# Kernel tuning notes

Measured on AMD Instinct MI355X. Metric: run time of the kernel, lower is better.

Reference implementation:

```python
import jax, jax.numpy as jnp
import numpy as np
from jax import lax

T, N, E = 12, 20000, 320000          # timesteps, nodes/graph, edges/graph
F_IN, H_GCN, H_LSTM, N_CLS = 128, 256, 256, 8
NUM_GRAPHS = 1                        # one graph per snapshot (batch all zeros)


def setup_inputs() -> dict:
    key = jax.random.key(0)
    ks = jax.random.split(key, 12)
    s = 0.05
    return {
        "x": jax.random.normal(ks[0], (T, N, F_IN), jnp.float32),
        "edge_index": jax.random.randint(ks[1], (T, 2, E), 0, N, dtype=jnp.int32),
        "batch": jnp.zeros((T, N), jnp.int32),
        "W1": jax.random.normal(ks[2], (F_IN, H_GCN), jnp.float32) * s,
        "b1": jnp.zeros((H_GCN,), jnp.float32),
        "W2": jax.random.normal(ks[3], (H_GCN, H_GCN), jnp.float32) * s,
        "b2": jnp.zeros((H_GCN,), jnp.float32),
        "Wih0": jax.random.normal(ks[4], (4 * H_LSTM, H_GCN), jnp.float32) * s,
        "Whh0": jax.random.normal(ks[5], (4 * H_LSTM, H_LSTM), jnp.float32) * s,
        "bih0": jnp.zeros((4 * H_LSTM,), jnp.float32),
        "bhh0": jnp.zeros((4 * H_LSTM,), jnp.float32),
        "Wih1": jax.random.normal(ks[6], (4 * H_LSTM, H_LSTM), jnp.float32) * s,
        "Whh1": jax.random.normal(ks[7], (4 * H_LSTM, H_LSTM), jnp.float32) * s,
        "bih1": jnp.zeros((4 * H_LSTM,), jnp.float32),
        "bhh1": jnp.zeros((4 * H_LSTM,), jnp.float32),
        "Wlin": jax.random.normal(ks[8], (N_CLS, H_LSTM), jnp.float32) * s,
        "blin": jnp.zeros((N_CLS,), jnp.float32),
    }


def gcn_conv(x, src, dst, W, b, n):
    """PyG GCNConv: linear -> add self-loops -> sym-norm gather/scale/scatter-add + bias."""
    loop = jnp.arange(n, dtype=src.dtype)
    src = jnp.concatenate([src, loop])
    dst = jnp.concatenate([dst, loop])
    deg = jax.ops.segment_sum(jnp.ones(dst.shape, x.dtype), dst, num_segments=n)
    dinv = jnp.where(deg > 0, lax.rsqrt(deg), 0.0)
    norm = dinv[src] * dinv[dst]                       # [E+N]
    xl = x @ W                                         # [N, H]
    out = jax.ops.segment_sum(xl[src] * norm[:, None], dst, num_segments=n)
    return out + b


def lstm_layer(xs, Wih, Whh, bih, bhh):
    """Single-direction LSTM over xs [T, D]; PyTorch gate order i,f,g,o."""
    H = Whh.shape[1]
    bias = bih + bhh

    def step(carry, x):
        h, c = carry
        gates = x @ Wih.T + h @ Whh.T + bias
        i, f, g, o = jnp.split(gates, 4, axis=-1)
        c = jax.nn.sigmoid(f) * c + jax.nn.sigmoid(i) * jnp.tanh(g)
        h = jax.nn.sigmoid(o) * jnp.tanh(c)
        return (h, c), h

    h0 = jnp.zeros((H,), xs.dtype)
    (_, _), hs = lax.scan(step, (h0, h0), xs)
    return hs


def reference(x, edge_index, batch, W1, b1, W2, b2,
              Wih0, Whh0, bih0, bhh0, Wih1, Whh1, bih1, bhh1, Wlin, blin):
    def gcn_step(_, inp):
        xt, et, bt = inp
        h = jax.nn.relu(gcn_conv(xt, et[0], et[1], W1, b1, N))
        h = jax.nn.relu(gcn_conv(h, et[0], et[1], W2, b2, N))
        sums = jax.ops.segment_sum(h, bt, num_segments=NUM_GRAPHS)
        cnt = jax.ops.segment_sum(jnp.ones((N,), h.dtype), bt, num_segments=NUM_GRAPHS)
        return 0, sums / cnt[:, None]                  # global_mean_pool -> [NUM_GRAPHS, H_GCN]

    _, pooled = lax.scan(gcn_step, 0, (x, edge_index, batch))
    seq = pooled.reshape(T * NUM_GRAPHS, H_GCN)        # cat(dim=0) of per-step embeddings
    h1 = lstm_layer(seq, Wih0, Whh0, bih0, bhh0)
    h2 = lstm_layer(h1, Wih1, Whh1, bih1, bhh1)
    return (h2[-1] @ Wlin.T + blin)[None, :]           # [1, N_CLS]
```

## Files before the change

### kernel.cpp

```cpp
#include <hip/hip_runtime.h>
#include <hip/hip_bf16.h>
#include <math.h>

#define T_STEPS 12
#define NNODES  20000
#define NEDGES  320000
#define MPAD    20032
#define FIN     128
#define HG      256
#define RS_STRIDE 20032
#define CHK     16
#define HALF    10000

typedef unsigned short u16;
typedef unsigned int   u32;
typedef unsigned char  u8;
typedef unsigned long long u64;
using bf16x8 = __attribute__((ext_vector_type(8))) short;
using f32x4  = __attribute__((ext_vector_type(4))) float;
typedef float v2f __attribute__((ext_vector_type(2)));

__device__ __forceinline__ float bf2f(u16 u) {
    union { u32 i; float f; } v; v.i = ((u32)u) << 16; return v.f;
}
__device__ __forceinline__ u16 f2bf(float f) {
    union { float f; u32 i; } v; v.f = f;
    u32 r = v.i + 0x7fffu + ((v.i >> 16) & 1u);
    return (u16)(r >> 16);
}
__device__ __forceinline__ u16 f2h(float f) {
    _Float16 h = (_Float16)f; u16 u; __builtin_memcpy(&u, &h, 2); return u;
}
__device__ __forceinline__ float h2f(u16 u) {
    _Float16 h; __builtin_memcpy(&h, &u, 2); return (float)h;
}
__device__ __forceinline__ void gload16(const void* g, void* l) {
    __builtin_amdgcn_global_load_lds(
        (const __attribute__((address_space(1))) u32*)g,
        (__attribute__((address_space(3))) u32*)l, 16, 0, 0);
}
__device__ __forceinline__ float sigm(float x) { return 1.f / (1.f + expf(-x)); }


__global__ void __launch_bounds__(1024) hist2(const int* __restrict__ edges,
        u8* __restrict__ rank, u8* __restrict__ counts) {
    __shared__ u32 lh[HALF];
    int c = blockIdx.x & 15;
    int rest = blockIdx.x >> 4;
    int s = rest & 1, t = rest >> 1;
    for (int i = threadIdx.x; i < HALF; i += 1024) lh[i] = 0;
    __syncthreads();
    int lo = s * HALF;
    const int* db = edges + (size_t)t * 2 * NEDGES + NEDGES;
    u8* rk = rank + (size_t)t * NEDGES;
    int per = NEDGES / CHK;
    int e0 = c * per, e1 = e0 + per;
    for (int i = e0 + (int)threadIdx.x; i < e1; i += 1024) {
        int d = db[i] - lo;
        if ((unsigned)d < HALF) {
            u32 r = atomicAdd(&lh[d], 1u);
            rk[i] = (u8)r;
        }
    }
    __syncthreads();
    u8* cnt = counts + (((size_t)(t * 2 + s) * CHK + c) * HALF);
    for (int i = threadIdx.x; i < HALF; i += 1024) cnt[i] = (u8)lh[i];
}

__global__ void __launch_bounds__(1024) scan2(const u8* __restrict__ counts,
        int* __restrict__ rowstart, float* __restrict__ dinv,
        int* __restrict__ chunkoff) {
    int t = blockIdx.x;
    int tid = threadIdx.x;
    int wid = tid >> 6, lane = tid & 63;
    __shared__ int wsum[16];
    __shared__ int carry_s;
    if (tid == 0) carry_s = 0;
    __syncthreads();
    for (int base = 0; base < NNODES; base += 1024) {
        int i = base + tid;
        int cl[CHK];
        int orig = 0;
        if (i < NNODES) {
            int s = i / HALF, np = i - s * HALF;
            const u8* cp = counts + ((size_t)(t * 2 + s) * CHK) * HALF + np;
#pragma unroll
            for (int c = 0; c < CHK; ++c) { cl[c] = cp[c * HALF]; orig += cl[c]; }
        }
        int v = orig;
#pragma unroll
        for (int off = 1; off < 64; off <<= 1) {
            int n = __shfl_up(v, off);
            if (lane >= off) v += n;
        }
        if (lane == 63) wsum[wid] = v;
        __syncthreads();
        if (wid == 0 && lane < 16) {
            int s = wsum[lane];
#pragma unroll
            for (int off = 1; off < 16; off <<= 1) {
                int n = __shfl_up(s, off);
                if (lane >= off) s += n;
            }
            wsum[lane] = s;
        }
        __syncthreads();
        int incl = v + (wid > 0 ? wsum[wid - 1] : 0) + carry_s;
        int excl = incl - orig;
        if (i < NNODES) {
            rowstart[t * RS_STRIDE + i] = excl;
            dinv[t * NNODES + i] = rsqrtf((float)(orig + 1));
            int s = i / HALF, np = i - s * HALF;
            int* op = chunkoff + ((size_t)(t * 2 + s) * CHK) * HALF + np;
            int run = excl;
#pragma unroll
            for (int c = 0; c < CHK; ++c) { op[c * HALF] = run; run += cl[c]; }
        }
        __syncthreads();
        if (tid == 0) carry_s += wsum[15];
        __syncthreads();
    }
    if (tid == 0) rowstart[t * RS_STRIDE + NNODES] = carry_s;
}

__global__ void __launch_bounds__(1024) fill2(const int* __restrict__ edges,
        const u8* __restrict__ rank, const int* __restrict__ chunkoff,
        int* __restrict__ col) {
    __shared__ int loff[HALF];
    int c = blockIdx.x & 15;
    int rest = blockIdx.x >> 4;
    int s = rest & 1, t = rest >> 1;
    const int* op = chunkoff + (((size_t)(t * 2 + s) * CHK + c) * HALF);
    for (int i = threadIdx.x; i < HALF; i += 1024) loff[i] = op[i];
    __syncthreads();
    int lo = s * HALF;
    const int* sb = edges + (size_t)t * 2 * NEDGES;
    const int* db = sb + NEDGES;
    const u8* rk = rank + (size_t)t * NEDGES;
    int* ct = col + (size_t)t * NEDGES;
    int per = NEDGES / CHK;
    int e0 = c * per, e1 = e0 + per;
    for (int i = e0 + (int)threadIdx.x; i < e1; i += 1024) {
        int d = db[i] - lo;
        if ((unsigned)d < HALF)
            ct[loff[d] + (int)rk[i]] = sb[i];
    }
}


__global__ void __launch_bounds__(256) convall(
        const float* __restrict__ x, const float* __restrict__ dinv, u8* __restrict__ xb,
        const float* __restrict__ W1, u16* __restrict__ W1t,
        const float* __restrict__ W2, u16* __restrict__ W2t,
        const float* __restrict__ Wih0, const float* __restrict__ Whh0,
        const float* __restrict__ Wih1, const float* __restrict__ Whh1,
        u32* __restrict__ lw,
        float* __restrict__ pooled, u64* __restrict__ hbuf) {
    int bid = blockIdx.x;
    int tid = threadIdx.x;
    if (bid < 30000) {
        int idx = bid * 256 + tid;
        int row = idx >> 5, q = idx & 31;
        float dn = dinv[row];
        float4 v = *(const float4*)&x[(size_t)row * FIN + q * 4];
        int p = __builtin_amdgcn_cvt_pk_fp8_f32(dn * v.x, dn * v.y, 0, false);
        p = __builtin_amdgcn_cvt_pk_fp8_f32(dn * v.z, dn * v.w, p, true);
        ((u32*)xb)[(size_t)row * 32 + q] = (u32)p;
    } else if (bid < 30128) {
        int idx = (bid - 30000) * 256 + tid;
        int n = idx / FIN, k = idx - n * FIN;
        W1t[idx] = f2bf(W1[k * HG + n]);
    } else if (bid < 30384) {
        int idx = (bid - 30128) * 256 + tid;
        int n = idx >> 8, k = idx & 255;
        W2t[idx] = f2bf(W2[k * HG + n]);
    } else if (bid == 30384) {
        for (int i = tid; i < T_STEPS * HG; i += 256) pooled[i] = 0.f;
        for (int i = tid; i < 256; i += 256) hbuf[i] = 0ull;
    } else {
        int idx = bid - 30385;
        int m = idx >> 10, r = idx & 1023;
        const float* src = (m == 0) ? Wih0 : (m == 1) ? Whh0 : (m == 2) ? Wih1 : Whh1;
        if (tid < 128) {
            float2 w2 = *(const float2*)&src[(size_t)r * HG + tid * 2];
            lw[((size_t)m * 128 + tid) * 1024 + r] =
                (u32)f2h(w2.x) | ((u32)f2h(w2.y) << 16);
        }
    }
}


__global__ void __launch_bounds__(256) agg128(const u8* __restrict__ xb,
        const int* __restrict__ rowstart, const int* __restrict__ col,
        const float* __restrict__ dinv, u16* __restrict__ out) {
    int glob = (blockIdx.x << 2) + (threadIdx.x >> 6);
    int lane = threadIdx.x & 63;
    int t = glob / MPAD, node = glob - t * MPAD;
    u16* orow = out + ((size_t)glob) * FIN;
    if (node >= NNODES) { *(u32*)&orow[lane << 1] = 0; return; }
    const u8* xt = xb + (size_t)t * NNODES * FIN;
    const int* cb = col + (size_t)t * NEDGES;
    int o2 = lane << 1;
    u32 pv = *(const u16*)&xt[(size_t)node * FIN + o2];
    v2f f = __builtin_amdgcn_cvt_pk_f32_fp8((int)pv, false);
    float ax = f[0], ay = f[1];
    int s0 = rowstart[t * RS_STRIDE + node], s1 = rowstart[t * RS_STRIDE + node + 1];
    int e = s0;
    for (; e + 16 <= s1; e += 16) {
        int ix[16]; u32 rv[16];
#pragma unroll
        for (int j = 0; j < 16; ++j) ix[j] = cb[e + j];
#pragma unroll
        for (int j = 0; j < 16; ++j) rv[j] = *(const u16*)&xt[(size_t)ix[j] * FIN + o2];
#pragma unroll
        for (int j = 0; j < 16; ++j) {
            v2f g = __builtin_amdgcn_cvt_pk_f32_fp8((int)rv[j], false);
            ax += g[0]; ay += g[1];
        }
    }
    for (; e + 4 <= s1; e += 4) {
        int ix[4]; u32 rv[4];
#pragma unroll
        for (int j = 0; j < 4; ++j) ix[j] = cb[e + j];
#pragma unroll
        for (int j = 0; j < 4; ++j) rv[j] = *(const u16*)&xt[(size_t)ix[j] * FIN + o2];
#pragma unroll
        for (int j = 0; j < 4; ++j) {
            v2f g = __builtin_amdgcn_cvt_pk_f32_fp8((int)rv[j], false);
            ax += g[0]; ay += g[1];
        }
    }
    for (; e < s1; ++e) {
        u32 rv = *(const u16*)&xt[(size_t)cb[e] * FIN + o2];
        v2f g = __builtin_amdgcn_cvt_pk_f32_fp8((int)rv, false);
        ax += g[0]; ay += g[1];
    }
    float dn = dinv[t * NNODES + node];
    u32 packed = (u32)f2bf(dn * ax) | ((u32)f2bf(dn * ay) << 16);
    *(u32*)&orow[o2] = packed;
}

__global__ void __launch_bounds__(256) agg256(const u8* __restrict__ xin,
        const int* __restrict__ rowstart, const int* __restrict__ col,
        const float* __restrict__ dinv, u16* __restrict__ out) {
    int glob = (blockIdx.x << 2) + (threadIdx.x >> 6);
    int lane = threadIdx.x & 63;
    int t = glob / MPAD, node = glob - t * MPAD;
    u16* orow = out + ((size_t)glob) * HG;
    if (node >= NNODES) { *(ushort4*)&orow[lane << 2] = make_ushort4(0, 0, 0, 0); return; }
    const u8* xt = xin + (size_t)t * MPAD * HG;
    const int* cb = col + (size_t)t * NEDGES;
    int o4 = lane << 2;
    u32 pv = *(const u32*)&xt[(size_t)node * HG + o4];
    v2f f01 = __builtin_amdgcn_cvt_pk_f32_fp8((int)pv, false);
    v2f f23 = __builtin_amdgcn_cvt_pk_f32_fp8((int)pv, true);
    float a0 = f01[0], a1 = f01[1], a2 = f23[0], a3 = f23[1];
    int s0 = rowstart[t * RS_STRIDE + node], s1 = rowstart[t * RS_STRIDE + node + 1];
    int e = s0;
    for (; e + 16 <= s1; e += 16) {
        int ix[16]; u32 rv[16];
#pragma unroll
        for (int j = 0; j < 16; ++j) ix[j] = cb[e + j];
#pragma unroll
        for (int j = 0; j < 16; ++j) rv[j] = *(const u32*)&xt[(size_t)ix[j] * HG + o4];
#pragma unroll
        for (int j = 0; j < 16; ++j) {
            v2f g01 = __builtin_amdgcn_cvt_pk_f32_fp8((int)rv[j], false);
            v2f g23 = __builtin_amdgcn_cvt_pk_f32_fp8((int)rv[j], true);
            a0 += g01[0]; a1 += g01[1]; a2 += g23[0]; a3 += g23[1];
        }
    }
    for (; e + 4 <= s1; e += 4) {
        int ix[4]; u32 rv[4];
#pragma unroll
        for (int j = 0; j < 4; ++j) ix[j] = cb[e + j];
#pragma unroll
        for (int j = 0; j < 4; ++j) rv[j] = *(const u32*)&xt[(size_t)ix[j] * HG + o4];
#pragma unroll
        for (int j = 0; j < 4; ++j) {
            v2f g01 = __builtin_amdgcn_cvt_pk_f32_fp8((int)rv[j], false);
            v2f g23 = __builtin_amdgcn_cvt_pk_f32_fp8((int)rv[j], true);
            a0 += g01[0]; a1 += g01[1]; a2 += g23[0]; a3 += g23[1];
        }
    }
    for (; e < s1; ++e) {
        u32 rv = *(const u32*)&xt[(size_t)cb[e] * HG + o4];
        v2f g01 = __builtin_amdgcn_cvt_pk_f32_fp8((int)rv, false);
        v2f g23 = __builtin_amdgcn_cvt_pk_f32_fp8((int)rv, true);
        a0 += g01[0]; a1 += g01[1]; a2 += g23[0]; a3 += g23[1];
    }
    float dn = dinv[t * NNODES + node];
    ushort4 o;
    o.x = f2bf(dn * a0); o.y = f2bf(dn * a1); o.z = f2bf(dn * a2); o.w = f2bf(dn * a3);
    *(ushort4*)&orow[o4] = o;
}


template <int K, bool POOL>
__global__ __launch_bounds__(256) void gemm_bf16(
        const u16* __restrict__ A, const u16* __restrict__ Bt,
        const float* __restrict__ bias, const float* __restrict__ dscale,
        u8* __restrict__ C, float* __restrict__ pool) {
    __shared__ u16 As[64 * 64];
    __shared__ u16 Bs[256 * 64];
    __shared__ float csum[HG];
    int tid = threadIdx.x;
    int bm = blockIdx.x * 64;
    int t8 = tid >> 3, sl = tid & 7;
    int lane = tid & 63, w = tid >> 6;
    int r0 = lane & 15, gq = lane >> 4;
    int tblk = blockIdx.x / 313;

    f32x4 acc[4][4] = {};

    for (int k0 = 0; k0 < K; k0 += 64) {
#pragma unroll
        for (int i = 0; i < 2; ++i) {
            int r = i * 32 + t8;
            int ch = sl ^ (r & 7);
            gload16(A + (size_t)(bm + r) * K + k0 + ch * 8, &As[i * 2048 + tid * 8]);
        }
#pragma unroll
        for (int i = 0; i < 8; ++i) {
            int r = i * 32 + t8;
            int ch = sl ^ (r & 7);
            gload16(Bt + (size_t)r * K + k0 + ch * 8, &Bs[i * 2048 + tid * 8]);
        }
        __syncthreads();
#pragma unroll
        for (int kk = 0; kk < 2; ++kk) {
            bf16x8 a[4], b[4];
#pragma unroll
            for (int mi = 0; mi < 4; ++mi) {
                int R = mi * 16 + r0;
                int s = (kk * 4 + gq) ^ (R & 7);
                a[mi] = *(const bf16x8*)&As[R * 64 + s * 8];
            }
#pragma unroll
            for (int ni = 0; ni < 4; ++ni) {
                int R = w * 64 + ni * 16 + r0;
                int s = (kk * 4 + gq) ^ (R & 7);
                b[ni] = *(const bf16x8*)&Bs[R * 64 + s * 8];
            }
#pragma unroll
            for (int mi = 0; mi < 4; ++mi)
#pragma unroll
                for (int ni = 0; ni < 4; ++ni)
                    acc[mi][ni] = __builtin_amdgcn_mfma_f32_16x16x32_bf16(
                        a[mi], b[ni], acc[mi][ni], 0, 0, 0);
        }
        __syncthreads();
    }

    if (!POOL) {
#pragma unroll
        for (int ni = 0; ni < 4; ++ni) {
            int colg = w * 64 + ni * 16 + r0;
            float b = bias[colg];
#pragma unroll
            for (int mi = 0; mi < 4; ++mi) {
                int rbase = bm + mi * 16 + gq * 4;
#pragma unroll
                for (int q = 0; q < 4; ++q) {
                    int row = rbase + q;
                    int rloc = row - tblk * MPAD;
                    float sc = (rloc < NNODES) ? dscale[tblk * NNODES + rloc] : 0.f;
                    float val = sc * fmaxf(acc[mi][ni][q] + b, 0.f);
                    int p = __builtin_amdgcn_cvt_pk_fp8_f32(val, val, 0, false);
                    C[(size_t)row * HG + colg] = (u8)(p & 0xff);
                }
            }
        }
    } else {
        csum[tid] = 0.f;
        __syncthreads();
#pragma unroll
        for (int ni = 0; ni < 4; ++ni) {
            int colg = w * 64 + ni * 16 + r0;
            float b = bias[colg];
            float s = 0.f;
#pragma unroll
            for (int mi = 0; mi < 4; ++mi) {
                int rbase = bm + mi * 16 + gq * 4;
#pragma unroll
                for (int q = 0; q < 4; ++q) {
                    int row = rbase + q;
                    int rloc = row - tblk * MPAD;
                    if (rloc < NNODES) s += fmaxf(acc[mi][ni][q] + b, 0.f);
                }
            }
            atomicAdd(&csum[colg], s);
        }
        __syncthreads();
        atomicAdd(&pool[tblk * HG + tid], csum[tid]);
    }
}


__global__ void __launch_bounds__(256, 1) lstm4d(
        const float* __restrict__ pooled, const u32* __restrict__ lw,
        const float* __restrict__ bih0, const float* __restrict__ bhh0,
        const float* __restrict__ bih1, const float* __restrict__ bhh1,
        const float* __restrict__ Wlin, const float* __restrict__ blin,
        u64* hbuf, float* __restrict__ out) {
    __shared__ float xs[T_STEPS][HG];
    __shared__ float hseqL[T_STEPS][HG];
    __shared__ float hl[HG];
    __shared__ float garr[256];
    int tid = threadIdx.x;
    int b = blockIdx.x;
    int lu = tid & 63;
    int unit = b * 64 + lu;
    int r = (tid >> 6) * 256 + unit;

    for (int i = tid; i < T_STEPS * HG; i += 256)
        ((float*)xs)[i] = pooled[i] * (1.f / (float)NNODES);
    __syncthreads();

    float pre[T_STEPS];
    {
        const u32* wp = lw + r;
#pragma unroll
        for (int t = 0; t < T_STEPS; ++t) pre[t] = 0.f;
        for (int k = 0; k < 128; ++k) {
            u32 pk = wp[(size_t)k * 1024];
            float w0 = h2f((u16)pk), w1 = h2f((u16)(pk >> 16));
#pragma unroll
            for (int t = 0; t < T_STEPS; ++t)
                pre[t] += w0 * xs[t][2 * k] + w1 * xs[t][2 * k + 1];
        }
        float bb = bih0[r] + bhh0[r];
#pragma unroll
        for (int t = 0; t < T_STEPS; ++t) pre[t] += bb;
    }

    u32 wreg[128];
    for (int layer = 0; layer < 2; ++layer) {
        {
            const u32* wp = lw + (size_t)((layer ? 3 : 1) * 128) * 1024 + r;
#pragma unroll
            for (int k = 0; k < 128; ++k) wreg[k] = wp[(size_t)k * 1024];
        }
        float c = 0.f;
        hl[tid] = 0.f;
        __syncthreads();
        for (int t = 0; t < T_STEPS; ++t) {
            int s = layer * T_STEPS + t + 1;
            float acc = 0.f;
#pragma unroll
            for (int k = 0; k < 128; ++k) {
                u32 wv = wreg[k];
                float2 hv = *(const float2*)&hl[k * 2];
                acc += h2f((u16)wv) * hv.x + h2f((u16)(wv >> 16)) * hv.y;
            }
            garr[tid] = pre[t] + acc;
            __syncthreads();
            if (tid < 64) {
                float ig = sigm(garr[lu]);
                float fg = sigm(garr[64 + lu]);
                float gg = tanhf(garr[128 + lu]);
                float og = sigm(garr[192 + lu]);
                c = fg * c + ig * gg;
                float hn = og * tanhf(c);
                u16 hb16 = f2bf(hn);
                hl[unit] = bf2f(hb16);
                if (lu < 32) {
                    u16 h0 = f2bf(hl[b * 64 + 2 * lu]);
                    u16 h1 = f2bf(hl[b * 64 + 2 * lu + 1]);
                    u64 pk = ((u64)(u32)s << 32) | (u32)h0 | ((u32)h1 << 16);
                    __hip_atomic_store(&hbuf[(s & 1) * 128 + b * 32 + lu], pk,
                                       __ATOMIC_RELAXED, __HIP_MEMORY_SCOPE_AGENT);
                }
            }
            if (tid < 128 && (tid >> 5) != b) {
                u64 v = __hip_atomic_load(&hbuf[(s & 1) * 128 + tid],
                                          __ATOMIC_RELAXED, __HIP_MEMORY_SCOPE_AGENT);
                while ((u32)(v >> 32) != (u32)s) {
                    __builtin_amdgcn_s_sleep(1);
                    v = __hip_atomic_load(&hbuf[(s & 1) * 128 + tid],
                                          __ATOMIC_RELAXED, __HIP_MEMORY_SCOPE_AGENT);
                }
                u32 lo = (u32)v;
                hl[2 * tid]     = bf2f((u16)lo);
                hl[2 * tid + 1] = bf2f((u16)(lo >> 16));
            }
            __syncthreads();
            if (layer == 0) hseqL[t][tid] = hl[tid];
        }
        if (layer == 0) {
            __syncthreads();
            const u32* wp = lw + (size_t)(2 * 128) * 1024 + r;
#pragma unroll
            for (int t = 0; t < T_STEPS; ++t) pre[t] = 0.f;
            for (int k = 0; k < 128; ++k) {
                u32 pk = wp[(size_t)k * 1024];
                float w0 = h2f((u16)pk), w1 = h2f((u16)(pk >> 16));
#pragma unroll
                for (int t = 0; t < T_STEPS; ++t)
                    pre[t] += w0 * hseqL[t][2 * k] + w1 * hseqL[t][2 * k + 1];
            }
            float bb = bih1[r] + bhh1[r];
#pragma unroll
            for (int t = 0; t < T_STEPS; ++t) pre[t] += bb;
            __syncthreads();
        }
    }

    if (b == 0 && tid < 8) {
        float s = blin[tid];
        const float* wl = Wlin + tid * HG;
        for (int k = 0; k < HG; ++k) s += hl[k] * wl[k];
        out[tid] = s;
    }
}


extern "C" void kernel_launch(void* const* d_in, const int* in_sizes, int n_in,
                              void* d_out, int out_size, void* d_ws, size_t ws_size,
                              hipStream_t stream) {
    const float* x    = (const float*)d_in[0];
    const int*   edges= (const int*)d_in[1];
    const float* W1   = (const float*)d_in[3];
    const float* b1   = (const float*)d_in[4];
    const float* W2   = (const float*)d_in[5];
    const float* b2   = (const float*)d_in[6];
    const float* Wih0 = (const float*)d_in[7];
    const float* Whh0 = (const float*)d_in[8];
    const float* bih0 = (const float*)d_in[9];
    const float* bhh0 = (const float*)d_in[10];
    const float* Wih1 = (const float*)d_in[11];
    const float* Whh1 = (const float*)d_in[12];
    const float* bih1 = (const float*)d_in[13];
    const float* bhh1 = (const float*)d_in[14];
    const float* Wlin = (const float*)d_in[15];
    const float* blin = (const float*)d_in[16];
    (void)in_sizes; (void)n_in; (void)out_size;

    char* p = (char*)d_ws;
    auto alloc = [&](size_t bytes) -> char* {
        char* q = p; p += (bytes + 255) & ~(size_t)255; return q;
    };
    int*   rowstart = (int*)  alloc(sizeof(int)   * T_STEPS * RS_STRIDE);
    float* dinv     = (float*)alloc(sizeof(float) * T_STEPS * NNODES);
    int*   col      = (int*)  alloc(sizeof(int)   * T_STEPS * NEDGES);
    u8*    rank     = (u8*)   alloc((size_t)T_STEPS * NEDGES);
    u8*    counts   = (u8*)   alloc((size_t)T_STEPS * 2 * CHK * HALF);
    int*   chunkoff = (int*)  alloc(sizeof(int)   * (size_t)T_STEPS * 2 * CHK * HALF);
    float* pooled   = (float*)alloc(sizeof(float) * T_STEPS * HG);
    u16*   W1t      = (u16*)  alloc(sizeof(u16)   * HG * FIN);
    u16*   W2t      = (u16*)  alloc(sizeof(u16)   * HG * HG);
    u32*   lw       = (u32*)  alloc(sizeof(u32)   * 4 * 128 * 1024);
    u64*   hbuf     = (u64*)  alloc(sizeof(u64)   * 2 * 128);
    size_t fixed_used = (size_t)(p - (char*)d_ws);

    const size_t xb_bytes  = (size_t)T_STEPS * NNODES * FIN;
    const size_t per_g     = (size_t)MPAD * HG * (1 + 2);
    const size_t slack     = 4096 * 16;
    static const int gopts[6] = {12, 6, 4, 3, 2, 1};
    int G = 1;
    for (int i = 0; i < 6; ++i)
        if (fixed_used + xb_bytes + per_g * gopts[i] + slack <= ws_size) { G = gopts[i]; break; }
    u8*  xb   = (u8*) alloc(xb_bytes);
    u8*  h1b  = (u8*) alloc((size_t)G * MPAD * HG);
    u16* aggu = (u16*)alloc(sizeof(u16) * (size_t)G * MPAD * HG);

    hist2<<<T_STEPS * 2 * CHK, 1024, 0, stream>>>(edges, rank, counts);
    scan2<<<T_STEPS, 1024, 0, stream>>>(counts, rowstart, dinv, chunkoff);
    fill2<<<T_STEPS * 2 * CHK, 1024, 0, stream>>>(edges, rank, chunkoff, col);
    convall<<<34481, 256, 0, stream>>>(x, dinv, xb, W1, W1t, W2, W2t,
                                       Wih0, Whh0, Wih1, Whh1, lw, pooled, hbuf);

    for (int g = 0; g < T_STEPS / G; ++g) {
        int t0 = g * G;
        const u8*    xbg = xb + (size_t)t0 * NNODES * FIN;
        const int*   rsg = rowstart + (size_t)t0 * RS_STRIDE;
        const int*   clg = col + (size_t)t0 * NEDGES;
        const float* dvg = dinv + (size_t)t0 * NNODES;
        int nagg = G * MPAD / 4;
        agg128<<<nagg, 256, 0, stream>>>(xbg, rsg, clg, dvg, aggu);
        gemm_bf16<FIN, false><<<G * 313, 256, 0, stream>>>(aggu, W1t, b1, dvg,
                h1b, nullptr);
        agg256<<<nagg, 256, 0, stream>>>(h1b, rsg, clg, dvg, aggu);
        gemm_bf16<HG, true><<<G * 313, 256, 0, stream>>>(aggu, W2t, b2, nullptr,
                nullptr, pooled + (size_t)t0 * HG);
    }
    lstm4d<<<4, 256, 0, stream>>>(pooled, lw, bih0, bhh0, bih1, bhh1, Wlin, blin,
                                  hbuf, (float*)d_out);
}
```

Before: 762.1 us.

## Split LSTM recurrence across two blocks with two gate rows per thread

The recurrent LSTM kernel drops from four cooperating blocks to two. Each thread now holds two gate rows of recurrent weights in registers, and hidden state is exchanged between blocks as full fp32 values, one per slot, through a larger flag-tagged buffer. This halves the number of cross-block participants in the per-step spin-wait handshake. In exchange, per-thread work and register pressure double (256 packed weight registers), which risks spills or longer per-step compute. Dropping the bf16 rounding of h also changes numerics slightly.

```diff
diff --git a/kernel.cpp b/kernel.cpp
--- a/kernel.cpp
+++ b/kernel.cpp
@@ -176,7 +176,7 @@
         W2t[idx] = f2bf(W2[k * HG + n]);
     } else if (bid == 30384) {
         for (int i = tid; i < T_STEPS * HG; i += 256) pooled[i] = 0.f;
-        for (int i = tid; i < 256; i += 256) hbuf[i] = 0ull;
+        for (int i = tid; i < 512; i += 256) hbuf[i] = 0ull;
     } else {
         int idx = bid - 30385;
         int m = idx >> 10, r = idx & 1023;
@@ -397,7 +397,7 @@
 }
 
 
-__global__ void __launch_bounds__(256, 1) lstm4d(
+__global__ void __launch_bounds__(256, 1) lstm2d(
         const float* __restrict__ pooled, const u32* __restrict__ lw,
         const float* __restrict__ bih0, const float* __restrict__ bhh0,
         const float* __restrict__ bih1, const float* __restrict__ bhh1,
@@ -406,102 +406,117 @@
     __shared__ float xs[T_STEPS][HG];
     __shared__ float hseqL[T_STEPS][HG];
     __shared__ float hl[HG];
-    __shared__ float garr[256];
+    __shared__ float garr[4][128];
     int tid = threadIdx.x;
-    int b = blockIdx.x;
-    int lu = tid & 63;
-    int unit = b * 64 + lu;
-    int r = (tid >> 6) * 256 + unit;
+    int b = blockIdx.x, ob = 1 - b;
+    int ul = tid & 127;
+    int u = b * 128 + ul;
+    int g0 = (tid >> 7) * 2;
+    int r0 = g0 * 256 + u, r1 = (g0 + 1) * 256 + u;
 
     for (int i = tid; i < T_STEPS * HG; i += 256)
         ((float*)xs)[i] = pooled[i] * (1.f / (float)NNODES);
     __syncthreads();
 
-    float pre[T_STEPS];
+    u32 wregA[128], wregB[128];
+    float preA[T_STEPS], preB[T_STEPS];
+
     {
-        const u32* wp = lw + r;
-#pragma unroll
-        for (int t = 0; t < T_STEPS; ++t) pre[t] = 0.f;
+        const u32* wpA = lw + r0;
+        const u32* wpB = lw + r1;
+#pragma unroll
+        for (int k = 0; k < 128; ++k) { wregA[k] = wpA[(size_t)k * 1024]; wregB[k] = wpB[(size_t)k * 1024]; }
+#pragma unroll
+        for (int t = 0; t < T_STEPS; ++t) { preA[t] = 0.f; preB[t] = 0.f; }
         for (int k = 0; k < 128; ++k) {
-            u32 pk = wp[(size_t)k * 1024];
-            float w0 = h2f((u16)pk), w1 = h2f((u16)(pk >> 16));
-#pragma unroll
-            for (int t = 0; t < T_STEPS; ++t)
-                pre[t] += w0 * xs[t][2 * k] + w1 * xs[t][2 * k + 1];
-        }
-        float bb = bih0[r] + bhh0[r];
-#pragma unroll
-        for (int t = 0; t < T_STEPS; ++t) pre[t] += bb;
-    }
-
-    u32 wreg[128];
+            u32 wa = wregA[k], wb = wregB[k];
+            float a0 = h2f((u16)wa), a1 = h2f((u16)(wa >> 16));
+            float b0 = h2f((u16)wb), b1 = h2f((u16)(wb >> 16));
+#pragma unroll
+            for (int t = 0; t < T_STEPS; ++t) {
+                float x0 = xs[t][2 * k], x1 = xs[t][2 * k + 1];
+                preA[t] += a0 * x0 + a1 * x1;
+                preB[t] += b0 * x0 + b1 * x1;
+            }
+        }
+        float bbA = bih0[r0] + bhh0[r0];
+        float bbB = bih0[r1] + bhh0[r1];
+#pragma unroll
+        for (int t = 0; t < T_STEPS; ++t) { preA[t] += bbA; preB[t] += bbB; }
+    }
+
+    float c = 0.f;
     for (int layer = 0; layer < 2; ++layer) {
         {
-            const u32* wp = lw + (size_t)((layer ? 3 : 1) * 128) * 1024 + r;
-#pragma unroll
-            for (int k = 0; k < 128; ++k) wreg[k] = wp[(size_t)k * 1024];
-        }
-        float c = 0.f;
+            const u32* wpA = lw + (size_t)((layer ? 3 : 1) * 128) * 1024 + r0;
+            const u32* wpB = lw + (size_t)((layer ? 3 : 1) * 128) * 1024 + r1;
+#pragma unroll
+            for (int k = 0; k < 128; ++k) { wregA[k] = wpA[(size_t)k * 1024]; wregB[k] = wpB[(size_t)k * 1024]; }
+        }
+        c = 0.f;
         hl[tid] = 0.f;
+        if (tid < 256 - HG) {  }
         __syncthreads();
         for (int t = 0; t < T_STEPS; ++t) {
             int s = layer * T_STEPS + t + 1;
-            float acc = 0.f;
+            float acc0 = 0.f, acc1 = 0.f;
 #pragma unroll
             for (int k = 0; k < 128; ++k) {
-                u32 wv = wreg[k];
+                u32 wa = wregA[k], wb = wregB[k];
                 float2 hv = *(const float2*)&hl[k * 2];
-                acc += h2f((u16)wv) * hv.x + h2f((u16)(wv >> 16)) * hv.y;
-            }
-            garr[tid] = pre[t] + acc;
+                acc0 += h2f((u16)wa) * hv.x + h2f((u16)(wa >> 16)) * hv.y;
+                acc1 += h2f((u16)wb) * hv.x + h2f((u16)(wb >> 16)) * hv.y;
+            }
+            garr[g0][ul]     = preA[t] + acc0;
+            garr[g0 + 1][ul] = preB[t] + acc1;
             __syncthreads();
-            if (tid < 64) {
-                float ig = sigm(garr[lu]);
-                float fg = sigm(garr[64 + lu]);
-                float gg = tanhf(garr[128 + lu]);
-                float og = sigm(garr[192 + lu]);
+            if (tid < 128) {
+                float ig = sigm(garr[0][tid]);
+                float fg = sigm(garr[1][tid]);
+                float gg = tanhf(garr[2][tid]);
+                float og = sigm(garr[3][tid]);
                 c = fg * c + ig * gg;
                 float hn = og * tanhf(c);
-                u16 hb16 = f2bf(hn);
-                hl[unit] = bf2f(hb16);
-                if (lu < 32) {
-                    u16 h0 = f2bf(hl[b * 64 + 2 * lu]);
-                    u16 h1 = f2bf(hl[b * 64 + 2 * lu + 1]);
-                    u64 pk = ((u64)(u32)s << 32) | (u32)h0 | ((u32)h1 << 16);
-                    __hip_atomic_store(&hbuf[(s & 1) * 128 + b * 32 + lu], pk,
-                                       __ATOMIC_RELAXED, __HIP_MEMORY_SCOPE_AGENT);
-                }
-            }
-            if (tid < 128 && (tid >> 5) != b) {
-                u64 v = __hip_atomic_load(&hbuf[(s & 1) * 128 + tid],
+                hl[u] = hn;
+                u32 hb; __builtin_memcpy(&hb, &hn, 4);
+                u64 pk = ((u64)(u32)s << 32) | (u64)hb;
+                __hip_atomic_store(&hbuf[(s & 1) * 256 + u], pk,
+                                   __ATOMIC_RELAXED, __HIP_MEMORY_SCOPE_AGENT);
+                u64 v = __hip_atomic_load(&hbuf[(s & 1) * 256 + ob * 128 + tid],
                                           __ATOMIC_RELAXED, __HIP_MEMORY_SCOPE_AGENT);
                 while ((u32)(v >> 32) != (u32)s) {
                     __builtin_amdgcn_s_sleep(1);
-                    v = __hip_atomic_load(&hbuf[(s & 1) * 128 + tid],
+                    v = __hip_atomic_load(&hbuf[(s & 1) * 256 + ob * 128 + tid],
                                           __ATOMIC_RELAXED, __HIP_MEMORY_SCOPE_AGENT);
                 }
                 u32 lo = (u32)v;
-                hl[2 * tid]     = bf2f((u16)lo);
-                hl[2 * tid + 1] = bf2f((u16)(lo >> 16));
+                float hv; __builtin_memcpy(&hv, &lo, 4);
+                hl[ob * 128 + tid] = hv;
             }
             __syncthreads();
             if (layer == 0) hseqL[t][tid] = hl[tid];
         }
         if (layer == 0) {
             __syncthreads();
-            const u32* wp = lw + (size_t)(2 * 128) * 1024 + r;
-#pragma unroll
-            for (int t = 0; t < T_STEPS; ++t) pre[t] = 0.f;
+            const u32* wpA = lw + (size_t)(2 * 128) * 1024 + r0;
+            const u32* wpB = lw + (size_t)(2 * 128) * 1024 + r1;
+#pragma unroll
+            for (int t = 0; t < T_STEPS; ++t) { preA[t] = 0.f; preB[t] = 0.f; }
             for (int k = 0; k < 128; ++k) {
-                u32 pk = wp[(size_t)k * 1024];
-                float w0 = h2f((u16)pk), w1 = h2f((u16)(pk >> 16));
-#pragma unroll
-                for (int t = 0; t < T_STEPS; ++t)
-                    pre[t] += w0 * hseqL[t][2 * k] + w1 * hseqL[t][2 * k + 1];
-            }
-            float bb = bih1[r] + bhh1[r];
-#pragma unroll
-            for (int t = 0; t < T_STEPS; ++t) pre[t] += bb;
+                u32 wa = wpA[(size_t)k * 1024], wb = wpB[(size_t)k * 1024];
+                float a0 = h2f((u16)wa), a1 = h2f((u16)(wa >> 16));
+                float b0 = h2f((u16)wb), b1 = h2f((u16)(wb >> 16));
+#pragma unroll
+                for (int t = 0; t < T_STEPS; ++t) {
+                    float h0 = hseqL[t][2 * k], h1 = hseqL[t][2 * k + 1];
+                    preA[t] += a0 * h0 + a1 * h1;
+                    preB[t] += b0 * h0 + b1 * h1;
+                }
+            }
+            float bbA = bih1[r0] + bhh1[r0];
+            float bbB = bih1[r1] + bhh1[r1];
+#pragma unroll
+            for (int t = 0; t < T_STEPS; ++t) { preA[t] += bbA; preB[t] += bbB; }
             __syncthreads();
         }
     }
@@ -550,7 +565,7 @@
     u16*   W1t      = (u16*)  alloc(sizeof(u16)   * HG * FIN);
     u16*   W2t      = (u16*)  alloc(sizeof(u16)   * HG * HG);
     u32*   lw       = (u32*)  alloc(sizeof(u32)   * 4 * 128 * 1024);
-    u64*   hbuf     = (u64*)  alloc(sizeof(u64)   * 2 * 128);
+    u64*   hbuf     = (u64*)  alloc(sizeof(u64)   * 2 * 256);
     size_t fixed_used = (size_t)(p - (char*)d_ws);
 
     const size_t xb_bytes  = (size_t)T_STEPS * NNODES * FIN;
@@ -584,6 +599,6 @@
         gemm_bf16<HG, true><<<G * 313, 256, 0, stream>>>(aggu, W2t, b2, nullptr,
                 nullptr, pooled + (size_t)t0 * HG);
     }
-    lstm4d<<<4, 256, 0, stream>>>(pooled, lw, bih0, bhh0, bih1, bhh1, Wlin, blin,
+    lstm2d<<<2, 256, 0, stream>>>(pooled, lw, bih0, bhh0, bih1, bhh1, Wlin, blin,
                                   hbuf, (float*)d_out);
 }
```

Measured after the change: 954.6 us. 1.25x slower.

## Pipeline the two LSTM layers across separate block groups

Applied to the files above, without the earlier changes.

The LSTM kernel now launches 8 blocks: four run layer 0 and four run layer 1 concurrently. Layer-0 hidden states go into a per-timestep global buffer, and layer 1 consumes each step as soon as it appears instead of waiting for the whole layer-0 sequence. Layer 1 keeps its input weights in shared memory and fuses the input and recurrent matvecs per step. Hidden states are also exchanged as fp32 rather than packed bf16, and the sleep in the spin-wait is dropped. This costs more global flag traffic and busy polling, and it depends on all 8 blocks being co-resident.

```diff
diff --git a/kernel.cpp b/kernel.cpp
--- a/kernel.cpp
+++ b/kernel.cpp
@@ -176,7 +176,7 @@
         W2t[idx] = f2bf(W2[k * HG + n]);
     } else if (bid == 30384) {
         for (int i = tid; i < T_STEPS * HG; i += 256) pooled[i] = 0.f;
-        for (int i = tid; i < 256; i += 256) hbuf[i] = 0ull;
+        for (int i = tid; i < (T_STEPS + 2) * 256; i += 256) hbuf[i] = 0ull;
     } else {
         int idx = bid - 30385;
         int m = idx >> 10, r = idx & 1023;
@@ -397,47 +397,49 @@
 }
 
 
-__global__ void __launch_bounds__(256, 1) lstm4d(
+__global__ void __launch_bounds__(256, 1) lstm_pipe(
         const float* __restrict__ pooled, const u32* __restrict__ lw,
         const float* __restrict__ bih0, const float* __restrict__ bhh0,
         const float* __restrict__ bih1, const float* __restrict__ bhh1,
         const float* __restrict__ Wlin, const float* __restrict__ blin,
         u64* hbuf, float* __restrict__ out) {
     __shared__ float xs[T_STEPS][HG];
-    __shared__ float hseqL[T_STEPS][HG];
+    __shared__ u32 wih[128][256];
     __shared__ float hl[HG];
+    __shared__ float h0l[HG];
     __shared__ float garr[256];
+    u64* hbuf0 = hbuf;
+    u64* hbuf1 = hbuf + T_STEPS * 256;
     int tid = threadIdx.x;
-    int b = blockIdx.x;
+    int L = blockIdx.x >> 2;
+    int b = blockIdx.x & 3;
     int lu = tid & 63;
     int unit = b * 64 + lu;
     int r = (tid >> 6) * 256 + unit;
-
-    for (int i = tid; i < T_STEPS * HG; i += 256)
-        ((float*)xs)[i] = pooled[i] * (1.f / (float)NNODES);
-    __syncthreads();
-
-    float pre[T_STEPS];
-    {
-        const u32* wp = lw + r;
-#pragma unroll
-        for (int t = 0; t < T_STEPS; ++t) pre[t] = 0.f;
-        for (int k = 0; k < 128; ++k) {
-            u32 pk = wp[(size_t)k * 1024];
-            float w0 = h2f((u16)pk), w1 = h2f((u16)(pk >> 16));
-#pragma unroll
-            for (int t = 0; t < T_STEPS; ++t)
-                pre[t] += w0 * xs[t][2 * k] + w1 * xs[t][2 * k + 1];
-        }
-        float bb = bih0[r] + bhh0[r];
-#pragma unroll
-        for (int t = 0; t < T_STEPS; ++t) pre[t] += bb;
-    }
-
     u32 wreg[128];
-    for (int layer = 0; layer < 2; ++layer) {
+
+    if (L == 0) {
+        for (int i = tid; i < T_STEPS * HG; i += 256)
+            ((float*)xs)[i] = pooled[i] * (1.f / (float)NNODES);
+        __syncthreads();
+        float pre[T_STEPS];
         {
-            const u32* wp = lw + (size_t)((layer ? 3 : 1) * 128) * 1024 + r;
+            const u32* wp = lw + r;
+#pragma unroll
+            for (int t = 0; t < T_STEPS; ++t) pre[t] = 0.f;
+            for (int k = 0; k < 128; ++k) {
+                u32 pk = wp[(size_t)k * 1024];
+                float w0 = h2f((u16)pk), w1 = h2f((u16)(pk >> 16));
+#pragma unroll
+                for (int t = 0; t < T_STEPS; ++t)
+                    pre[t] += w0 * xs[t][2 * k] + w1 * xs[t][2 * k + 1];
+            }
+            float bb = bih0[r] + bhh0[r];
+#pragma unroll
+            for (int t = 0; t < T_STEPS; ++t) pre[t] += bb;
+        }
+        {
+            const u32* wp = lw + (size_t)128 * 1024 + r;
 #pragma unroll
             for (int k = 0; k < 128; ++k) wreg[k] = wp[(size_t)k * 1024];
         }
@@ -445,7 +447,7 @@
         hl[tid] = 0.f;
         __syncthreads();
         for (int t = 0; t < T_STEPS; ++t) {
-            int s = layer * T_STEPS + t + 1;
+            int s = t + 1;
             float acc = 0.f;
 #pragma unroll
             for (int k = 0; k < 128; ++k) {
@@ -462,55 +464,92 @@
                 float og = sigm(garr[192 + lu]);
                 c = fg * c + ig * gg;
                 float hn = og * tanhf(c);
-                u16 hb16 = f2bf(hn);
-                hl[unit] = bf2f(hb16);
-                if (lu < 32) {
-                    u16 h0 = f2bf(hl[b * 64 + 2 * lu]);
-                    u16 h1 = f2bf(hl[b * 64 + 2 * lu + 1]);
-                    u64 pk = ((u64)(u32)s << 32) | (u32)h0 | ((u32)h1 << 16);
-                    __hip_atomic_store(&hbuf[(s & 1) * 128 + b * 32 + lu], pk,
-                                       __ATOMIC_RELAXED, __HIP_MEMORY_SCOPE_AGENT);
-                }
-            }
-            if (tid < 128 && (tid >> 5) != b) {
-                u64 v = __hip_atomic_load(&hbuf[(s & 1) * 128 + tid],
+                u32 hb; __builtin_memcpy(&hb, &hn, 4);
+                u64 pk = ((u64)(u32)s << 32) | (u64)hb;
+                __hip_atomic_store(&hbuf0[t * 256 + unit], pk,
+                                   __ATOMIC_RELAXED, __HIP_MEMORY_SCOPE_AGENT);
+            }
+            if (t < T_STEPS - 1) {
+                u64 v;
+                do {
+                    v = __hip_atomic_load(&hbuf0[t * 256 + tid],
                                           __ATOMIC_RELAXED, __HIP_MEMORY_SCOPE_AGENT);
-                while ((u32)(v >> 32) != (u32)s) {
-                    __builtin_amdgcn_s_sleep(1);
-                    v = __hip_atomic_load(&hbuf[(s & 1) * 128 + tid],
+                } while ((u32)(v >> 32) != (u32)s);
+                u32 lo = (u32)v;
+                float hv; __builtin_memcpy(&hv, &lo, 4);
+                __syncthreads();
+                hl[tid] = hv;
+                __syncthreads();
+            }
+        }
+    } else {
+        for (int k = 0; k < 128; ++k)
+            wih[k][tid] = lw[((size_t)(2 * 128) + k) * 1024 + r];
+        {
+            const u32* wp = lw + (size_t)(3 * 128) * 1024 + r;
+#pragma unroll
+            for (int k = 0; k < 128; ++k) wreg[k] = wp[(size_t)k * 1024];
+        }
+        float bias1 = bih1[r] + bhh1[r];
+        float c = 0.f;
+        hl[tid] = 0.f;
+        __syncthreads();
+        for (int t = 0; t < T_STEPS; ++t) {
+            int s = t + 1;
+            {
+                u64 v;
+                do {
+                    v = __hip_atomic_load(&hbuf0[t * 256 + tid],
                                           __ATOMIC_RELAXED, __HIP_MEMORY_SCOPE_AGENT);
-                }
+                } while ((u32)(v >> 32) != (u32)s);
                 u32 lo = (u32)v;
-                hl[2 * tid]     = bf2f((u16)lo);
-                hl[2 * tid + 1] = bf2f((u16)(lo >> 16));
+                float hv; __builtin_memcpy(&hv, &lo, 4);
+                h0l[tid] = hv;
             }
             __syncthreads();
-            if (layer == 0) hseqL[t][tid] = hl[tid];
-        }
-        if (layer == 0) {
+            float acc = 0.f;
+#pragma unroll
+            for (int k = 0; k < 128; ++k) {
+                u32 wi = wih[k][tid];
+                u32 wh = wreg[k];
+                float2 h0v = *(const float2*)&h0l[k * 2];
+                float2 h1v = *(const float2*)&hl[k * 2];
+                acc += h2f((u16)wi) * h0v.x + h2f((u16)(wi >> 16)) * h0v.y
+                     + h2f((u16)wh) * h1v.x + h2f((u16)(wh >> 16)) * h1v.y;
+            }
+            garr[tid] = acc + bias1;
             __syncthreads();
-            const u32* wp = lw + (size_t)(2 * 128) * 1024 + r;
-#pragma unroll
-            for (int t = 0; t < T_STEPS; ++t) pre[t] = 0.f;
-            for (int k = 0; k < 128; ++k) {
-                u32 pk = wp[(size_t)k * 1024];
-                float w0 = h2f((u16)pk), w1 = h2f((u16)(pk >> 16));
-#pragma unroll
-                for (int t = 0; t < T_STEPS; ++t)
-                    pre[t] += w0 * hseqL[t][2 * k] + w1 * hseqL[t][2 * k + 1];
-            }
-            float bb = bih1[r] + bhh1[r];
-#pragma unroll
-            for (int t = 0; t < T_STEPS; ++t) pre[t] += bb;
-            __syncthreads();
-        }
-    }
-
-    if (b == 0 && tid < 8) {
-        float s = blin[tid];
-        const float* wl = Wlin + tid * HG;
-        for (int k = 0; k < HG; ++k) s += hl[k] * wl[k];
-        out[tid] = s;
+            if (tid < 64) {
+                float ig = sigm(garr[lu]);
+                float fg = sigm(garr[64 + lu]);
+                float gg = tanhf(garr[128 + lu]);
+                float og = sigm(garr[192 + lu]);
+                c = fg * c + ig * gg;
+                float hn = og * tanhf(c);
+                u32 hb; __builtin_memcpy(&hb, &hn, 4);
+                u64 pk = ((u64)(u32)s << 32) | (u64)hb;
+                __hip_atomic_store(&hbuf1[(s & 1) * 256 + unit], pk,
+                                   __ATOMIC_RELAXED, __HIP_MEMORY_SCOPE_AGENT);
+            }
+            {
+                u64 v;
+                do {
+                    v = __hip_atomic_load(&hbuf1[(s & 1) * 256 + tid],
+                                          __ATOMIC_RELAXED, __HIP_MEMORY_SCOPE_AGENT);
+                } while ((u32)(v >> 32) != (u32)s);
+                u32 lo = (u32)v;
+                float hv; __builtin_memcpy(&hv, &lo, 4);
+                __syncthreads();
+                hl[tid] = hv;
+                __syncthreads();
+            }
+        }
+        if (b == 0 && tid < 8) {
+            float sum = blin[tid];
+            const float* wl = Wlin + tid * HG;
+            for (int k = 0; k < HG; ++k) sum += hl[k] * wl[k];
+            out[tid] = sum;
+        }
     }
 }
 
@@ -550,7 +589,7 @@
     u16*   W1t      = (u16*)  alloc(sizeof(u16)   * HG * FIN);
     u16*   W2t      = (u16*)  alloc(sizeof(u16)   * HG * HG);
     u32*   lw       = (u32*)  alloc(sizeof(u32)   * 4 * 128 * 1024);
-    u64*   hbuf     = (u64*)  alloc(sizeof(u64)   * 2 * 128);
+    u64*   hbuf     = (u64*)  alloc(sizeof(u64)   * (T_STEPS + 2) * 256);
     size_t fixed_used = (size_t)(p - (char*)d_ws);
 
     const size_t xb_bytes  = (size_t)T_STEPS * NNODES * FIN;
@@ -584,6 +623,6 @@
         gemm_bf16<HG, true><<<G * 313, 256, 0, stream>>>(aggu, W2t, b2, nullptr,
                 nullptr, pooled + (size_t)t0 * HG);
     }
-    lstm4d<<<4, 256, 0, stream>>>(pooled, lw, bih0, bhh0, bih1, bhh1, Wlin, blin,
-                                  hbuf, (float*)d_out);
-}
+    lstm_pipe<<<8, 256, 0, stream>>>(pooled, lw, bih0, bhh0, bih1, bhh1, Wlin, blin,
+                                     hbuf, (float*)d_out);
+}
```

Measured after the change: 739.9 us. -2.9%, faster.
